# Performance work log

Measured on AMD Instinct MI355X. Metric: run time of the kernel, lower is better.

The kernel has to match this reference:

```python
import jax, jax.numpy as jnp
import numpy as np

DIM = 128
SQRT_DIM = float(np.sqrt(DIM))


def setup_inputs() -> dict:
    key = jax.random.key(0)
    k1, k2, k3, k4 = jax.random.split(key, 4)
    B, S, D = 16, 2048, DIM
    return {
        "query": jax.random.normal(k1, (B, S, D), dtype=jnp.float32),
        "key": jax.random.normal(k2, (B, S, D), dtype=jnp.float32),
        "value": jax.random.normal(k3, (B, S, D), dtype=jnp.float32),
        "trust_score": jax.random.uniform(k4, (B, 1, S), dtype=jnp.float32, minval=0.05, maxval=1.0),
    }


def reference(query, key, value, trust_score):
    # score: [B, q, k]
    score = jnp.einsum("bqd,bkd->bqk", query, key) / SQRT_DIM
    score = score * trust_score
    attn = jax.nn.softmax(score, axis=-1)
    # trust reweighting + renormalization
    attn = attn * trust_score
    attn = attn / jnp.sum(attn, axis=-1, keepdims=True)
    context = jnp.einsum("bqk,bkd->bqd", attn, value)
    return context
```

## Files before the change

### kernel.cpp

```cpp
#include <hip/hip_runtime.h>
#include <math.h>

#define SEQ 2048
#define DIM 128
#define KVB 32
#define NTILES (SEQ / KVB)
#define NT2 (NTILES / 2)
#define KTB 8192
#define VTB 8192

typedef __attribute__((ext_vector_type(8))) short bf16x8;
typedef __attribute__((ext_vector_type(16))) float f32x16;
typedef __attribute__((ext_vector_type(4))) short short4v;
typedef __attribute__((ext_vector_type(4))) float f32x4;

union frag_u { bf16x8 h; unsigned u[4]; };

__device__ __forceinline__ short f2bf(float f) {
  union { float f; unsigned u; } v; v.f = f;
  unsigned r = v.u + 0x7FFFu + ((v.u >> 16) & 1u);
  return (short)(r >> 16);
}
__device__ __forceinline__ float bf2f(short h) {
  return __uint_as_float(((unsigned)(unsigned short)h) << 16);
}
__device__ __forceinline__ unsigned cvtpk(float lo, float hi) {
  unsigned r;
  asm("v_cvt_pk_bf16_f32 %0, %1, %2" : "=v"(r) : "v"(lo), "v"(hi));
  return r;
}
__device__ __forceinline__ void pl32swap(unsigned& a, unsigned& b) {
  asm("v_permlane32_swap_b32 %0, %1" : "+v"(a), "+v"(b));
}

__global__ __launch_bounds__(256)
void prepack_kernel(const float* __restrict__ Kg, const float* __restrict__ Vg,
                    const float* __restrict__ Tg,
                    char* __restrict__ Kws, char* __restrict__ Vws,
                    unsigned* __restrict__ Lws) {
  const int tile = blockIdx.x, b = blockIdx.y;
  const int tid = (int)threadIdx.x;
  const float* Kb = Kg + ((size_t)b * SEQ + tile * KVB) * DIM;
  const float* Vb = Vg + ((size_t)b * SEQ + tile * KVB) * DIM;
  const float* Tb = Tg + (size_t)b * SEQ + tile * KVB;
  char* kd = Kws + (size_t)(b * NTILES + tile) * KTB;
  char* vd = Vws + (size_t)(b * NTILES + tile) * VTB;

  #pragma unroll
  for (int i = 0; i < 2; ++i) {
    int id = i * 256 + tid;
    int c = id >> 6, l = id & 63;
    int hi = l >> 5, k = l & 31;
    int dstart = (2 * c + hi) * 8;
    float sc = Tb[k] * 0.12751743f;
    const float4 f0 = *(const float4*)(Kb + (size_t)k * DIM + dstart);
    const float4 f1 = *(const float4*)(Kb + (size_t)k * DIM + dstart + 4);
    bf16x8 pk;
    pk[0]=f2bf(f0.x*sc); pk[1]=f2bf(f0.y*sc); pk[2]=f2bf(f0.z*sc); pk[3]=f2bf(f0.w*sc);
    pk[4]=f2bf(f1.x*sc); pk[5]=f2bf(f1.y*sc); pk[6]=f2bf(f1.z*sc); pk[7]=f2bf(f1.w*sc);
    *(bf16x8*)(kd + id * 16) = pk;
  }
  #pragma unroll
  for (int i = 0; i < 2; ++i) {
    int id = i * 256 + tid;
    int g = id >> 6, l = id & 63;
    int hi = l >> 5, l31 = l & 31;
    int d = (g >> 1) * 32 + l31;
    int kstart = (2 * (g & 1) + hi) * 8;
    const float* src = Vb + (size_t)kstart * DIM + d;
    bf16x8 pk;
    #pragma unroll
    for (int j = 0; j < 8; ++j) pk[j] = f2bf(src[(size_t)j * DIM]);
    *(bf16x8*)(vd + id * 16) = pk;
  }
  if (tid < KVB) {
    float t = Tb[tid];
    float lt = log2f(t);
    short h = f2bf(lt);
    short lo = f2bf(lt - bf2f(h));
    Lws[(size_t)b * SEQ + tile * KVB + tid] =
        (unsigned)(unsigned short)h | ((unsigned)(unsigned short)lo << 16);
  }
}

__global__ __launch_bounds__(256, 2)
void trust_attn_main(const float* __restrict__ Qg, const char* __restrict__ Kws,
                     const char* __restrict__ Vws, const unsigned* __restrict__ Lws,
                     float* __restrict__ Og, int swz) {
  __shared__ __align__(16) char smem[33280];

  const int bid = (int)blockIdx.x;
  int b, qblk;
  if (swz) { int xcd = bid & 7, idx = bid >> 3; b = xcd * 2 + (idx >> 5); qblk = idx & 31; }
  else     { b = bid >> 5; qblk = bid & 31; }

  const int tid = (int)threadIdx.x;
  const int h   = tid >> 7;
  const int gq  = (tid >> 6) & 1;
  const int l   = tid & 63;
  const int hi  = l >> 5, l31 = l & 31;
  const int qcol = qblk * 64 + gq * 32 + l31;

  const float* Qr = Qg + ((size_t)b * SEQ + qcol) * DIM;
  const char* Kt = Kws + (size_t)(b * NTILES + h * NT2) * KTB + l * 16;
  const char* Vt = Vws + (size_t)(b * NTILES + h * NT2) * VTB + l * 16;
  const unsigned* Lb = Lws + (size_t)b * SEQ + h * (NT2 * KVB);

  frag_u qf[8];
  #pragma unroll
  for (int c = 0; c < 8; ++c) {
    const float4 a = *(const float4*)(Qr + c * 16 + hi * 8);
    const float4 d = *(const float4*)(Qr + c * 16 + hi * 8 + 4);
    bf16x8 q8;
    q8[0]=f2bf(a.x); q8[1]=f2bf(a.y); q8[2]=f2bf(a.z); q8[3]=f2bf(a.w);
    q8[4]=f2bf(d.x); q8[5]=f2bf(d.y); q8[6]=f2bf(d.z); q8[7]=f2bf(d.w);
    qf[c].h = q8;
  }
  frag_u qpad;
  qpad.u[0] = (hi == 0) ? 0x3F803F80u : 0u;
  qpad.u[1] = qpad.u[2] = qpad.u[3] = 0u;

  f32x16 acc[4];
  #pragma unroll
  for (int nt = 0; nt < 4; ++nt)
    #pragma unroll
    for (int i = 0; i < 16; ++i) acc[nt][i] = 0.f;
  float lsum = 0.f;

  frag_u kf[8], vf[8];
  #pragma unroll
  for (int c = 0; c < 8; ++c) kf[c].h = *(const bf16x8*)(Kt + c * 1024);
  #pragma unroll
  for (int g = 0; g < 8; ++g) vf[g].h = *(const bf16x8*)(Vt + g * 1024);
  unsigned ltc = Lb[l31];

  for (int t = 0; t < NT2; ++t) {
    const char* Kn = Kt + (size_t)(t + 1) * KTB;
    const char* Vn = Vt + (size_t)(t + 1) * VTB;

    f32x16 S0, S1;
    #pragma unroll
    for (int i = 0; i < 16; ++i) { S0[i] = 0.f; S1[i] = 0.f; }
    __builtin_amdgcn_s_setprio(1);
    #pragma unroll
    for (int c = 0; c < 8; c += 2) {
      S0 = __builtin_amdgcn_mfma_f32_32x32x16_bf16(kf[c].h, qf[c].h, S0, 0, 0, 0);
      S1 = __builtin_amdgcn_mfma_f32_32x32x16_bf16(kf[c + 1].h, qf[c + 1].h, S1, 0, 0, 0);
    }
    frag_u pa;
    pa.u[0] = (hi == 0) ? ltc : 0u;
    pa.u[1] = pa.u[2] = pa.u[3] = 0u;
    S1 = __builtin_amdgcn_mfma_f32_32x32x16_bf16(pa.h, qpad.h, S1, 0, 0, 0);
    __builtin_amdgcn_s_setprio(0);

    unsigned ltn = 0;
    if (t + 1 < NT2) {
      #pragma unroll
      for (int c = 0; c < 8; ++c) kf[c].h = *(const bf16x8*)(Kn + c * 1024);
      ltn = Lb[(t + 1) * KVB + l31];
    }

    float p[16];
    #pragma unroll
    for (int i = 0; i < 16; ++i) {
      p[i] = __builtin_amdgcn_exp2f(S0[i] + S1[i]);
      lsum += p[i];
    }

    frag_u PA[2];
    #pragma unroll
    for (int ks = 0; ks < 2; ++ks) {
      unsigned a0 = cvtpk(p[8*ks+0], p[8*ks+1]);
      unsigned a1 = cvtpk(p[8*ks+2], p[8*ks+3]);
      unsigned b0 = cvtpk(p[8*ks+4], p[8*ks+5]);
      unsigned b1 = cvtpk(p[8*ks+6], p[8*ks+7]);
      pl32swap(a0, b0);
      pl32swap(a1, b1);
      PA[ks].u[0] = a0; PA[ks].u[1] = a1; PA[ks].u[2] = b0; PA[ks].u[3] = b1;
    }

    __builtin_amdgcn_s_setprio(1);
    #pragma unroll
    for (int nt = 0; nt < 4; ++nt)
      #pragma unroll
      for (int ks = 0; ks < 2; ++ks)
        acc[nt] = __builtin_amdgcn_mfma_f32_32x32x16_bf16(vf[nt * 2 + ks].h, PA[ks].h, acc[nt], 0, 0, 0);
    __builtin_amdgcn_s_setprio(0);

    if (t + 1 < NT2) {
      #pragma unroll
      for (int g = 0; g < 8; ++g) vf[g].h = *(const bf16x8*)(Vn + g * 1024);
    }
    ltc = ltn;
  }

  const float Z = lsum + __shfl_xor(lsum, 32);
  float* AccX = (float*)smem;
  float* Zx   = (float*)(smem + 32768);
  const int q2 = gq * 32 + l31;

  __syncthreads();
  if (h == 1) {
    if (hi == 0) Zx[q2] = Z;
    #pragma unroll
    for (int nt = 0; nt < 4; ++nt)
      #pragma unroll
      for (int j = 0; j < 4; ++j) {
        int d = nt * 32 + j * 8 + hi * 4;
        int byte_off = (q2 * 512 + d * 4) ^ ((l31 & 7) << 4);
        f32x4 qd;
        qd[0] = acc[nt][j*4+0]; qd[1] = acc[nt][j*4+1];
        qd[2] = acc[nt][j*4+2]; qd[3] = acc[nt][j*4+3];
        *(f32x4*)((char*)AccX + byte_off) = qd;
      }
  }
  __syncthreads();
  if (h == 0) {
    const float inv = 1.0f / (Z + Zx[q2]);
    float* orow = Og + ((size_t)b * SEQ + qcol) * DIM;
    #pragma unroll
    for (int nt = 0; nt < 4; ++nt)
      #pragma unroll
      for (int j = 0; j < 4; ++j) {
        int d = nt * 32 + j * 8 + hi * 4;
        int byte_off = (q2 * 512 + d * 4) ^ ((l31 & 7) << 4);
        f32x4 o = *(const f32x4*)((const char*)AccX + byte_off);
        float4 r;
        r.x = (acc[nt][j*4+0] + o[0]) * inv;
        r.y = (acc[nt][j*4+1] + o[1]) * inv;
        r.z = (acc[nt][j*4+2] + o[2]) * inv;
        r.w = (acc[nt][j*4+3] + o[3]) * inv;
        *(float4*)(orow + d) = r;
      }
  }
}

__global__ __launch_bounds__(256, 2)
void trust_attn_fallback(const float* __restrict__ Qg, const float* __restrict__ Kg,
                         const float* __restrict__ Vg, const float* __restrict__ Tg,
                         float* __restrict__ Og) {
  __shared__ short Klds[2][64 * DIM];
  __shared__ short Vlds[2][DIM * 64];
  __shared__ short Plds[4][16 * 64];
  __shared__ float Tlds[2][64];

  const int b = blockIdx.y;
  const int qbase = blockIdx.x * 64;
  const int tid = (int)threadIdx.x;
  const int w = tid >> 6;
  const int l = tid & 63;
  const int lr = l & 15;
  const int lg = l >> 4;

  const float* Qb = Qg + (size_t)b * SEQ * DIM;
  const float* Kb = Kg + (size_t)b * SEQ * DIM;
  const float* Vb = Vg + (size_t)b * SEQ * DIM;
  const float* Tb = Tg + (size_t)b * SEQ;
  float*       Ob = Og + (size_t)b * SEQ * DIM;

  float4 kreg[8];
  float  vreg[32];
  float  treg;

  auto ISSUE = [&](int kv0) {
    #pragma unroll
    for (int i = 0; i < 8; ++i) {
      int flat4 = i * 256 + tid;
      int r = flat4 >> 5;
      int c4 = (flat4 & 31) << 2;
      kreg[i] = *(const float4*)(Kb + (size_t)(kv0 + r) * DIM + c4);
    }
    #pragma unroll
    for (int i = 0; i < 4; ++i) {
      int task = i * 256 + tid;
      int d = task & 127;
      int chunk = task >> 7;
      const float* src = Vb + (size_t)(kv0 + chunk * 8) * DIM + d;
      #pragma unroll
      for (int j = 0; j < 8; ++j) vreg[i * 8 + j] = src[(size_t)j * DIM];
    }
    treg = (tid < 64) ? Tb[kv0 + tid] : 0.f;
  };

  auto STORE = [&](int buf) {
    #pragma unroll
    for (int i = 0; i < 8; ++i) {
      int flat4 = i * 256 + tid;
      int r = flat4 >> 5;
      int c4 = (flat4 & 31) << 2;
      short4v pk;
      pk[0] = f2bf(kreg[i].x); pk[1] = f2bf(kreg[i].y);
      pk[2] = f2bf(kreg[i].z); pk[3] = f2bf(kreg[i].w);
      int byte_off = (r * 256 + (c4 << 1)) ^ ((r & 7) << 4);
      *(short4v*)((char*)&Klds[buf][0] + byte_off) = pk;
    }
    #pragma unroll
    for (int i = 0; i < 4; ++i) {
      int task = i * 256 + tid;
      int d = task & 127;
      int chunk = task >> 7;
      bf16x8 pk;
      #pragma unroll
      for (int j = 0; j < 8; ++j) pk[j] = f2bf(vreg[i * 8 + j]);
      int byte_off = (d * 128 + chunk * 16) ^ ((d & 7) << 4);
      *(bf16x8*)((char*)&Vlds[buf][0] + byte_off) = pk;
    }
    if (tid < 64) Tlds[buf][tid] = treg;
  };

  bf16x8 qf[4];
  {
    const float* qrow = Qb + (size_t)(qbase + w * 16 + lr) * DIM;
    #pragma unroll
    for (int kk = 0; kk < 4; ++kk) {
      const float4 a = *(const float4*)(qrow + kk * 32 + lg * 8);
      const float4 c = *(const float4*)(qrow + kk * 32 + lg * 8 + 4);
      bf16x8 f;
      f[0] = f2bf(a.x); f[1] = f2bf(a.y); f[2] = f2bf(a.z); f[3] = f2bf(a.w);
      f[4] = f2bf(c.x); f[5] = f2bf(c.y); f[6] = f2bf(c.z); f[7] = f2bf(c.w);
      qf[kk] = f;
    }
  }

  f32x4 acc[8];
  #pragma unroll
  for (int nt = 0; nt < 8; ++nt) acc[nt] = f32x4{0.f, 0.f, 0.f, 0.f};
  float lsum[4] = {0.f, 0.f, 0.f, 0.f};

  ISSUE(0);
  STORE(0);
  __syncthreads();

  for (int t = 0; t < SEQ / 64; ++t) {
    const int cur = t & 1;
    if (t + 1 < SEQ / 64) ISSUE((t + 1) * 64);

    const short* Kc = &Klds[cur][0];
    const short* Vc = &Vlds[cur][0];

    f32x4 s[4];
    #pragma unroll
    for (int kt = 0; kt < 4; ++kt) {
      f32x4 a0 = f32x4{0.f, 0.f, 0.f, 0.f};
      #pragma unroll
      for (int kk = 0; kk < 4; ++kk) {
        int row = kt * 16 + lr;
        int byte_off = (row * 256 + ((kk * 32 + lg * 8) << 1)) ^ ((row & 7) << 4);
        bf16x8 kf = *(const bf16x8*)((const char*)Kc + byte_off);
        a0 = __builtin_amdgcn_mfma_f32_16x16x32_bf16(qf[kk], kf, a0, 0, 0, 0);
      }
      s[kt] = a0;
    }

    short* Pw = Plds[w];
    #pragma unroll
    for (int kt = 0; kt < 4; ++kt) {
      float tt = Tlds[cur][kt * 16 + lr];
      float tc = tt * 0.12751743f;
      #pragma unroll
      for (int r = 0; r < 4; ++r) {
        float p = tt * exp2f(s[kt][r] * tc);
        lsum[r] += p;
        int q = lg * 4 + r;
        int byte_off = ((q * 128) + ((kt * 16 + lr) << 1)) ^ ((q & 7) << 4);
        *(short*)((char*)Pw + byte_off) = f2bf(p);
      }
    }
    asm volatile("s_waitcnt lgkmcnt(0)" ::: "memory");

    #pragma unroll
    for (int ks = 0; ks < 2; ++ks) {
      int byteA = (lr * 128 + ((ks * 32 + lg * 8) << 1)) ^ ((lr & 7) << 4);
      bf16x8 pf = *(const bf16x8*)((char*)Pw + byteA);
      #pragma unroll
      for (int nt = 0; nt < 8; ++nt) {
        int row = nt * 16 + lr;
        int byteB = (row * 128 + ((ks * 32 + lg * 8) << 1)) ^ ((row & 7) << 4);
        bf16x8 vf = *(const bf16x8*)((const char*)Vc + byteB);
        acc[nt] = __builtin_amdgcn_mfma_f32_16x16x32_bf16(pf, vf, acc[nt], 0, 0, 0);
      }
    }

    if (t + 1 < SEQ / 64) {
      STORE(cur ^ 1);
      __syncthreads();
    }
  }

  #pragma unroll
  for (int r = 0; r < 4; ++r) {
    float v = lsum[r];
    v += __shfl_xor(v, 1);
    v += __shfl_xor(v, 2);
    v += __shfl_xor(v, 4);
    v += __shfl_xor(v, 8);
    float inv = 1.0f / v;
    float* dst = Ob + (size_t)(qbase + w * 16 + lg * 4 + r) * DIM + lr;
    #pragma unroll
    for (int nt = 0; nt < 8; ++nt)
      dst[nt * 16] = acc[nt][r] * inv;
  }
}

extern "C" void kernel_launch(void* const* d_in, const int* in_sizes, int n_in,
                              void* d_out, int out_size, void* d_ws, size_t ws_size,
                              hipStream_t stream) {
  (void)n_in; (void)out_size;
  const float* Q = (const float*)d_in[0];
  const float* K = (const float*)d_in[1];
  const float* V = (const float*)d_in[2];
  const float* T = (const float*)d_in[3];
  float* O = (float*)d_out;
  const int B = in_sizes[0] / (SEQ * DIM);

  const size_t kv_bytes = (size_t)B * NTILES * KTB;
  const size_t need = kv_bytes * 2 + (size_t)B * SEQ * sizeof(unsigned);
  if (ws_size >= need) {
    char* Kws = (char*)d_ws;
    char* Vws = Kws + kv_bytes;
    unsigned* Lws = (unsigned*)(Vws + kv_bytes);
    dim3 gridp(NTILES, B);
    prepack_kernel<<<gridp, 256, 0, stream>>>(K, V, T, Kws, Vws, Lws);
    const int nblk = B * (SEQ / 64);
    const int swz = (B == 16) ? 1 : 0;
    trust_attn_main<<<nblk, 256, 0, stream>>>(Q, Kws, Vws, Lws, O, swz);
  } else {
    dim3 grid(SEQ / 64, B);
    trust_attn_fallback<<<grid, 256, 0, stream>>>(Q, K, V, T, O);
  }
}
```

Measured before the change: 67.55 us.

## Split KV sequence four ways per block with 32-query blocks and LDS reduction

Each block now handles 32 queries instead of 64, and its four waves each take a quarter of the KV tiles rather than two wave pairs each taking a half. This doubles the grid size and raises the launch bound to 3 blocks per CU, aiming for higher occupancy and better latency hiding. The partial accumulators and row sums are merged through a two-stage LDS reduction, with all four waves then writing the normalized output. In exchange, each wave has a shorter KV loop, there is an extra barrier and more LDS traffic, Q is loaded by more blocks, and register pressure may spill under the tighter launch bound.

```diff
diff --git a/kernel.cpp b/kernel.cpp
--- a/kernel.cpp
+++ b/kernel.cpp
@@ -5,7 +5,7 @@
 #define DIM 128
 #define KVB 32
 #define NTILES (SEQ / KVB)
-#define NT2 (NTILES / 2)
+#define NT4 (NTILES / 4)
 #define KTB 8192
 #define VTB 8192
 
@@ -83,7 +83,7 @@
   }
 }
 
-__global__ __launch_bounds__(256, 2)
+__global__ __launch_bounds__(256, 3)
 void trust_attn_main(const float* __restrict__ Qg, const char* __restrict__ Kws,
                      const char* __restrict__ Vws, const unsigned* __restrict__ Lws,
                      float* __restrict__ Og, int swz) {
@@ -91,20 +91,19 @@
 
   const int bid = (int)blockIdx.x;
   int b, qblk;
-  if (swz) { int xcd = bid & 7, idx = bid >> 3; b = xcd * 2 + (idx >> 5); qblk = idx & 31; }
-  else     { b = bid >> 5; qblk = bid & 31; }
+  if (swz) { int xcd = bid & 7, idx = bid >> 3; b = xcd * 2 + (idx >> 6); qblk = idx & 63; }
+  else     { b = bid >> 6; qblk = bid & 63; }
 
   const int tid = (int)threadIdx.x;
-  const int h   = tid >> 7;
-  const int gq  = (tid >> 6) & 1;
+  const int w   = tid >> 6;
   const int l   = tid & 63;
   const int hi  = l >> 5, l31 = l & 31;
-  const int qcol = qblk * 64 + gq * 32 + l31;
+  const int qcol = qblk * 32 + l31;
 
   const float* Qr = Qg + ((size_t)b * SEQ + qcol) * DIM;
-  const char* Kt = Kws + (size_t)(b * NTILES + h * NT2) * KTB + l * 16;
-  const char* Vt = Vws + (size_t)(b * NTILES + h * NT2) * VTB + l * 16;
-  const unsigned* Lb = Lws + (size_t)b * SEQ + h * (NT2 * KVB);
+  const char* Kt = Kws + (size_t)(b * NTILES + w * NT4) * KTB + l * 16;
+  const char* Vt = Vws + (size_t)(b * NTILES + w * NT4) * VTB + l * 16;
+  const unsigned* Lb = Lws + (size_t)b * SEQ + w * (NT4 * KVB);
 
   frag_u qf[8];
   #pragma unroll
@@ -132,11 +131,9 @@
   for (int c = 0; c < 8; ++c) kf[c].h = *(const bf16x8*)(Kt + c * 1024);
   #pragma unroll
   for (int g = 0; g < 8; ++g) vf[g].h = *(const bf16x8*)(Vt + g * 1024);
-  unsigned ltc = Lb[l31];
-
-  for (int t = 0; t < NT2; ++t) {
-    const char* Kn = Kt + (size_t)(t + 1) * KTB;
-    const char* Vn = Vt + (size_t)(t + 1) * VTB;
+
+  for (int t = 0; t < NT4; ++t) {
+    const unsigned ltc = Lb[t * KVB + l31];
 
     f32x16 S0, S1;
     #pragma unroll
@@ -153,11 +150,10 @@
     S1 = __builtin_amdgcn_mfma_f32_32x32x16_bf16(pa.h, qpad.h, S1, 0, 0, 0);
     __builtin_amdgcn_s_setprio(0);
 
-    unsigned ltn = 0;
-    if (t + 1 < NT2) {
-      #pragma unroll
-      for (int c = 0; c < 8; ++c) kf[c].h = *(const bf16x8*)(Kn + c * 1024);
-      ltn = Lb[(t + 1) * KVB + l31];
+    if (t + 1 < NT4) {
+      #pragma unroll
+      for (int c = 0; c < 8; ++c)
+        kf[c].h = *(const bf16x8*)(Kt + (size_t)(t + 1) * KTB + c * 1024);
     }
 
     float p[16];
@@ -187,51 +183,70 @@
         acc[nt] = __builtin_amdgcn_mfma_f32_32x32x16_bf16(vf[nt * 2 + ks].h, PA[ks].h, acc[nt], 0, 0, 0);
     __builtin_amdgcn_s_setprio(0);
 
-    if (t + 1 < NT2) {
-      #pragma unroll
-      for (int g = 0; g < 8; ++g) vf[g].h = *(const bf16x8*)(Vn + g * 1024);
-    }
-    ltc = ltn;
+    if (t + 1 < NT4) {
+      #pragma unroll
+      for (int g = 0; g < 8; ++g)
+        vf[g].h = *(const bf16x8*)(Vt + (size_t)(t + 1) * VTB + g * 1024);
+    }
   }
 
   const float Z = lsum + __shfl_xor(lsum, 32);
-  float* AccX = (float*)smem;
-  float* Zx   = (float*)(smem + 32768);
-  const int q2 = gq * 32 + l31;
-
-  __syncthreads();
-  if (h == 1) {
-    if (hi == 0) Zx[q2] = Z;
+  float* A0 = (float*)smem;
+  float* A1 = (float*)(smem + 16384);
+  float* Zx = (float*)(smem + 32768);
+  const int q2 = l31;
+
+  if (w < 2) {
+    float* A = (w == 0) ? A0 : A1;
+    if (hi == 0) Zx[w * 32 + q2] = Z;
     #pragma unroll
     for (int nt = 0; nt < 4; ++nt)
       #pragma unroll
       for (int j = 0; j < 4; ++j) {
         int d = nt * 32 + j * 8 + hi * 4;
-        int byte_off = (q2 * 512 + d * 4) ^ ((l31 & 7) << 4);
+        int byte_off = (q2 * 512 + d * 4) ^ ((q2 & 7) << 4);
         f32x4 qd;
         qd[0] = acc[nt][j*4+0]; qd[1] = acc[nt][j*4+1];
         qd[2] = acc[nt][j*4+2]; qd[3] = acc[nt][j*4+3];
-        *(f32x4*)((char*)AccX + byte_off) = qd;
+        *(f32x4*)((char*)A + byte_off) = qd;
       }
   }
   __syncthreads();
-  if (h == 0) {
-    const float inv = 1.0f / (Z + Zx[q2]);
-    float* orow = Og + ((size_t)b * SEQ + qcol) * DIM;
+  if (w >= 2) {
+    float* A = (w == 2) ? A0 : A1;
+    if (hi == 0) Zx[w * 32 + q2] = Z;
     #pragma unroll
     for (int nt = 0; nt < 4; ++nt)
       #pragma unroll
       for (int j = 0; j < 4; ++j) {
         int d = nt * 32 + j * 8 + hi * 4;
-        int byte_off = (q2 * 512 + d * 4) ^ ((l31 & 7) << 4);
-        f32x4 o = *(const f32x4*)((const char*)AccX + byte_off);
-        float4 r;
-        r.x = (acc[nt][j*4+0] + o[0]) * inv;
-        r.y = (acc[nt][j*4+1] + o[1]) * inv;
-        r.z = (acc[nt][j*4+2] + o[2]) * inv;
-        r.w = (acc[nt][j*4+3] + o[3]) * inv;
-        *(float4*)(orow + d) = r;
+        int byte_off = (q2 * 512 + d * 4) ^ ((q2 & 7) << 4);
+        f32x4 o = *(const f32x4*)((const char*)A + byte_off);
+        o[0] += acc[nt][j*4+0]; o[1] += acc[nt][j*4+1];
+        o[2] += acc[nt][j*4+2]; o[3] += acc[nt][j*4+3];
+        *(f32x4*)((char*)A + byte_off) = o;
       }
+  }
+  __syncthreads();
+  {
+    const int q = l31;
+    const float z = Zx[q] + Zx[32 + q] + Zx[64 + q] + Zx[96 + q];
+    const float inv = 1.0f / z;
+    float* orow = Og + ((size_t)b * SEQ + qblk * 32 + q) * DIM;
+    const int d0 = w * 32 + hi * 16;
+    #pragma unroll
+    for (int j = 0; j < 4; ++j) {
+      int d = d0 + j * 4;
+      int byte_off = (q * 512 + d * 4) ^ ((q & 7) << 4);
+      f32x4 a0 = *(const f32x4*)((const char*)A0 + byte_off);
+      f32x4 a1 = *(const f32x4*)((const char*)A1 + byte_off);
+      float4 r;
+      r.x = (a0[0] + a1[0]) * inv;
+      r.y = (a0[1] + a1[1]) * inv;
+      r.z = (a0[2] + a1[2]) * inv;
+      r.w = (a0[3] + a1[3]) * inv;
+      *(float4*)(orow + d) = r;
+    }
   }
 }
 
@@ -421,7 +436,7 @@
     unsigned* Lws = (unsigned*)(Vws + kv_bytes);
     dim3 gridp(NTILES, B);
     prepack_kernel<<<gridp, 256, 0, stream>>>(K, V, T, Kws, Vws, Lws);
-    const int nblk = B * (SEQ / 64);
+    const int nblk = B * 64;
     const int swz = (B == 16) ? 1 : 0;
     trust_attn_main<<<nblk, 256, 0, stream>>>(Q, Kws, Vws, Lws, O, swz);
   } else {
```

Measured after the change: 182.3 us. 2.7x slower.
